# Optimization experiments

Measured on AMD Instinct MI355X. Metric: run time of the kernel, lower is better.

The kernel has to match this reference:

```python
import jax, jax.numpy as jnp
import numpy as np

FILTER_SIZE = 1024
NUM_HEADS = 16
D_HEAD = FILTER_SIZE // NUM_HEADS
LN_EPS = 1e-5


def setup_inputs() -> dict:
    key = jax.random.key(0)
    ks = jax.random.split(key, 10)
    B, T, D = 2, 2048, FILTER_SIZE
    s = 1.0 / np.sqrt(D)
    return {
        "x": jax.random.normal(ks[0], (B, T, D), dtype=jnp.float32),
        "Wq": jax.random.normal(ks[1], (D, D), dtype=jnp.float32) * s,
        "bq": jnp.zeros((D,), dtype=jnp.float32),
        "Wk": jax.random.normal(ks[2], (D, D), dtype=jnp.float32) * s,
        "bk": jnp.zeros((D,), dtype=jnp.float32),
        "Wv": jax.random.normal(ks[3], (D, D), dtype=jnp.float32) * s,
        "bv": jnp.zeros((D,), dtype=jnp.float32),
        "Wo": jax.random.normal(ks[4], (D, D), dtype=jnp.float32) * s,
        "bo": jnp.zeros((D,), dtype=jnp.float32),
        "gamma": jnp.ones((D,), dtype=jnp.float32),
        "beta": jnp.zeros((D,), dtype=jnp.float32),
    }


def reference(x, Wq, bq, Wk, bk, Wv, bv, Wo, bo, gamma, beta):
    B, T, D = x.shape
    H, Dh = NUM_HEADS, D_HEAD
    # Note: source splits features as (d_head, heads) with heads LAST.
    q = (x @ Wq.T + bq).reshape(B, T, Dh, H)
    k = (x @ Wk.T + bk).reshape(B, T, Dh, H)
    v = (x @ Wv.T + bv).reshape(B, T, Dh, H)
    scale = 1.0 / np.sqrt(Dh).astype(np.float32)
    # scores: (B, H, T, T)
    scores = jnp.einsum("bidh,bjdh->bhij", q, k) * scale
    attn = jax.nn.softmax(scores, axis=-1)  # dropout is identity in eval
    out = jnp.einsum("bhij,bjdh->bidh", attn, v)  # (B, T, Dh, H)
    out = out.reshape(B, T, D)  # matches permute(0,2,3,1).reshape in torch
    out = out @ Wo.T + bo
    out = out + x
    mu = jnp.mean(out, axis=-1, keepdims=True)
    var = jnp.var(out, axis=-1, keepdims=True)
    out = (out - mu) * jax.lax.rsqrt(var + LN_EPS) * gamma + beta
    return out
```

## Files before the change

kernel.cpp:

```cpp
#include <hip/hip_runtime.h>
#include <stdint.h>

#define T_SEQ 2048
#define D_MODEL 1024
#define NH 16
#define DH 64
#define NROWS 4096

typedef __bf16 bf16x8 __attribute__((ext_vector_type(8)));
typedef float floatx4 __attribute__((ext_vector_type(4)));
typedef short short4v __attribute__((ext_vector_type(4)));
typedef short short8v __attribute__((ext_vector_type(8)));

#define AS1 __attribute__((address_space(1)))
#define AS3 __attribute__((address_space(3)))

static __device__ __forceinline__ void gl2lds16(const unsigned short* g, unsigned short* s) {
    __builtin_amdgcn_global_load_lds((const AS1 unsigned int*)g, (AS3 unsigned int*)s, 16, 0, 0);
}

static __device__ __forceinline__ unsigned short f32_bf16(float f) {
    union { float f; unsigned int u; } c; c.f = f;
    unsigned int u = c.u;
    u = u + 0x7FFFu + ((u >> 16) & 1u);
    return (unsigned short)(u >> 16);
}

static __device__ __forceinline__ unsigned int pack2_bf16(float a, float b) {
    return (unsigned int)f32_bf16(a) | ((unsigned int)f32_bf16(b) << 16);
}

static __device__ __forceinline__ floatx4 mfma16(bf16x8 a, bf16x8 b, floatx4 c) {
    return __builtin_amdgcn_mfma_f32_16x16x32_bf16(a, b, c, 0, 0, 0);
}

static __device__ __forceinline__ floatx4 mfma16k16(short4v a, short4v b, floatx4 c) {
#if defined(__HIP_DEVICE_COMPILE__)
    return __builtin_amdgcn_mfma_f32_16x16x16bf16_1k(a, b, c, 0, 0, 0);
#else
    (void)a; (void)b;
    return c;
#endif
}

#define QSCALE 0.1803368801111204f
#define EXP2_SHIFT 10.0f
#define WAITCNT_VM(n) (0x0F70 | (n))

__global__ __launch_bounds__(256) void k_conv_all(const float* __restrict__ x,
                                                  const float* __restrict__ Wq,
                                                  const float* __restrict__ Wk,
                                                  const float* __restrict__ Wv,
                                                  const float* __restrict__ Wo,
                                                  unsigned short* __restrict__ x_bf,
                                                  unsigned short* __restrict__ wqkv_bf,
                                                  unsigned short* __restrict__ wo_bf) {
    int b = blockIdx.x, t = threadIdx.x;
    if (b < 4096) {
        int i = b * 1024 + t * 4;
        float4 v = *(const float4*)(x + i);
        uint2 o;
        o.x = pack2_bf16(v.x, v.y);
        o.y = pack2_bf16(v.z, v.w);
        *(uint2*)(x_bf + i) = o;
    } else if (b < 7168) {
        int idx = b - 4096;
        int tensor = idx >> 10, np = idx & 1023;
        const float* src = tensor == 0 ? Wq : tensor == 1 ? Wk : Wv;
        int f = (np & 63) * 16 + (np >> 6);
        int c = t * 4;
        float4 v = *(const float4*)(src + (long)f * D_MODEL + c);
        uint2 o;
        o.x = pack2_bf16(v.x, v.y);
        o.y = pack2_bf16(v.z, v.w);
        *(uint2*)(wqkv_bf + ((long)tensor * D_MODEL + np) * D_MODEL + c) = o;
    } else {
        int n = b - 7168;
        int fp = t * 4;
        const float* row = Wo + (long)n * D_MODEL;
        unsigned short o[4];
        #pragma unroll
        for (int k = 0; k < 4; k++) {
            int f = fp + k;
            o[k] = f32_bf16(row[(f & 63) * 16 + (f >> 6)]);
        }
        *(uint2*)(wo_bf + (long)n * D_MODEL + fp) = *(const uint2*)o;
    }
}

template <int BN, int MODE>
__global__ __launch_bounds__(256) void k_gemm(const unsigned short* __restrict__ A,
                                              const unsigned short* __restrict__ W,
                                              const float* __restrict__ b0,
                                              const float* __restrict__ b1,
                                              const float* __restrict__ b2,
                                              const float* __restrict__ resid,
                                              unsigned short* __restrict__ out_bf,
                                              unsigned short* __restrict__ vtg,
                                              float* __restrict__ out_f32) {
    constexpr int NT = BN / 32;
    constexpr int NCB = BN / 32;
    constexpr int NDMA = 4 + NCB;
    __shared__ unsigned short lds_a[2 * 128 * 64];
    __shared__ unsigned short lds_b[2 * BN * 64];
    const int tid = threadIdx.x;
    const int w = tid >> 6, l = tid & 63;
    const int lrow = l & 15, lq = l >> 4;
    const int wm = (w >> 1) * 64, wn = (w & 1) * (BN / 2);
    const int L = blockIdx.x;
    const int bx = (L & 7) * 4 + ((L >> 3) & 3);
    const int by = L >> 5;
    const long am0 = (long)bx * 128;
    const long wn0 = (long)by * BN;

    floatx4 acc[4][NT] = {};
    const int grow = l >> 3;
    const int gcol = ((l & 7) ^ grow) * 8;
    const int sw8 = (lrow & 7);

    auto stage = [&](int ki, int sel) {
        unsigned short* la = lds_a + sel * 8192;
        unsigned short* lb = lds_b + sel * (BN * 64);
        int k0 = ki * 64;
        #pragma unroll
        for (int c = 0; c < 4; c++) {
            int chunk = w * 4 + c;
            gl2lds16(A + (am0 + chunk * 8 + grow) * D_MODEL + k0 + gcol, la + chunk * 512);
        }
        #pragma unroll
        for (int c = 0; c < NCB; c++) {
            int chunk = w * NCB + c;
            gl2lds16(W + (wn0 + chunk * 8 + grow) * D_MODEL + k0 + gcol, lb + chunk * 512);
        }
    };

    stage(0, 0);

    for (int i = 0; i < 16; i++) {
        const int cur = i & 1;
        if (i < 15) {
            stage(i + 1, 1 - cur);
            __builtin_amdgcn_s_waitcnt(WAITCNT_VM(NDMA));
        } else {
            __builtin_amdgcn_s_waitcnt(WAITCNT_VM(0));
        }
        __builtin_amdgcn_s_barrier();

        const unsigned short* la = lds_a + cur * 8192;
        const unsigned short* lb = lds_b + cur * (BN * 64);
        bf16x8 af[4][2], bf[NT][2];
        #pragma unroll
        for (int mt = 0; mt < 4; mt++)
            #pragma unroll
            for (int ks = 0; ks < 2; ks++)
                af[mt][ks] = *(const bf16x8*)(la + (wm + mt * 16 + lrow) * 64 +
                                              (((ks * 4 + lq) ^ sw8) * 8));
        #pragma unroll
        for (int nt = 0; nt < NT; nt++)
            #pragma unroll
            for (int ks = 0; ks < 2; ks++)
                bf[nt][ks] = *(const bf16x8*)(lb + (wn + nt * 16 + lrow) * 64 +
                                              (((ks * 4 + lq) ^ sw8) * 8));
        #pragma unroll
        for (int mt = 0; mt < 4; mt++)
            #pragma unroll
            for (int nt = 0; nt < NT; nt++)
                #pragma unroll
                for (int ks = 0; ks < 2; ks++)
                    acc[mt][nt] = mfma16(af[mt][ks], bf[nt][ks], acc[mt][nt]);
        __builtin_amdgcn_s_barrier();
    }

    if (MODE == 0) {
        int tensor = by >> 3;
        int nbase = (by & 7) * 128;
        const float* bias = tensor == 0 ? b0 : tensor == 1 ? b1 : b2;
        float scale = tensor == 0 ? QSCALE : 1.0f;
        if (tensor < 2) {
            unsigned short* outt = out_bf + (size_t)tensor * (32u * T_SEQ * DH);
            #pragma unroll
            for (int mt = 0; mt < 4; mt++) {
                #pragma unroll
                for (int nt = 0; nt < NT; nt++) {
                    int n = nbase + wn + nt * 16 + lrow;
                    int h = n >> 6, d = n & 63;
                    float bb = bias[d * 16 + h];
                    #pragma unroll
                    for (int r = 0; r < 4; r++) {
                        int row = (int)am0 + wm + mt * 16 + lq * 4 + r;
                        float v = (acc[mt][nt][r] + bb) * scale;
                        int b = row >> 11, i = row & 2047;
                        long idx = ((long)(b * 16 + h) * T_SEQ + i) * DH + d;
                        outt[idx] = f32_bf16(v);
                    }
                }
            }
        } else {
            int row0 = (int)am0 + wm;
            int b = row0 >> 11;
            int blk = (row0 & 2047) >> 6;
            #pragma unroll
            for (int nt = 0; nt < NT; nt++) {
                int n = nbase + wn + nt * 16 + lrow;
                int h = n >> 6, d = n & 63;
                float bb = bias[d * 16 + h];
                long base = (((long)(b * 16 + h) * 64 + d) * 32 + blk) * 64;
                #pragma unroll
                for (int mt = 0; mt < 4; mt++) {
                    uint2 o;
                    o.x = pack2_bf16(acc[mt][nt][0] + bb, acc[mt][nt][1] + bb);
                    o.y = pack2_bf16(acc[mt][nt][2] + bb, acc[mt][nt][3] + bb);
                    *(uint2*)(vtg + base + lq * 16 + mt * 4) = o;
                }
            }
        }
    } else {
        #pragma unroll
        for (int mt = 0; mt < 4; mt++) {
            #pragma unroll
            for (int nt = 0; nt < NT; nt++) {
                int n = (int)wn0 + wn + nt * 16 + lrow;
                float bb = b0[n];
                #pragma unroll
                for (int r = 0; r < 4; r++) {
                    int row = (int)am0 + wm + mt * 16 + lq * 4 + r;
                    long idx = (long)row * D_MODEL + n;
                    out_f32[idx] = acc[mt][nt][r] + bb + resid[idx];
                }
            }
        }
    }
}

__global__ __launch_bounds__(256) void k_attn(const unsigned short* __restrict__ q_ws,
                                              const unsigned short* __restrict__ k_ws,
                                              const unsigned short* __restrict__ vtg,
                                              unsigned short* __restrict__ att) {
    __shared__ unsigned short kbuf[2 * 64 * 64];
    __shared__ unsigned short vbuf[2 * 64 * 64];
    const int tid = threadIdx.x;
    const int w = tid >> 6, l = tid & 63;
    const int lrow = l & 15, lq = l >> 4;
    const int sw = lrow & 7;
    const int L = blockIdx.x;
    const int bh = (L & 7) * 4 + ((L >> 3) & 3);
    const int i0 = (L >> 5) * 128;
    const unsigned short* kh = k_ws + (long)bh * T_SEQ * DH;
    const unsigned short* vh = vtg + (long)bh * 64 * T_SEQ;

    const int rl = l >> 3;
    const int gl = ((l & 7) ^ rl) * 8;

    bf16x8 qf[2][2];
    #pragma unroll
    for (int qt = 0; qt < 2; qt++) {
        const unsigned short* qp =
            q_ws + ((long)bh * T_SEQ + i0 + w * 32 + qt * 16 + lrow) * DH + lq * 8;
        qf[qt][0] = *(const bf16x8*)qp;
        qf[qt][1] = *(const bf16x8*)(qp + 32);
    }
    floatx4 o_acc[2][4] = {};
    floatx4 l_acc[2] = {};
    const short4v ones = {0x3F80, 0x3F80, 0x3F80, 0x3F80};

    auto stage = [&](int jt, int sel) {
        unsigned short* kd = kbuf + sel * 4096 + (w * 2) * 512;
        unsigned short* vd = vbuf + sel * 4096 + (w * 2) * 512;
        #pragma unroll
        for (int c = 0; c < 2; c++) {
            int row = w * 16 + c * 8 + rl;
            gl2lds16(kh + ((long)(jt * 64 + row)) * 64 + gl, kd + c * 512);
            gl2lds16(vh + ((long)row * 32 + jt) * 64 + gl, vd + c * 512);
        }
    };

    stage(0, 0);

    constexpr int NTILE = T_SEQ / 64;
    for (int jt = 0; jt < NTILE; jt++) {
        const int cur = jt & 1;
        if (jt < NTILE - 1) {
            stage(jt + 1, 1 - cur);
            __builtin_amdgcn_s_waitcnt(WAITCNT_VM(4));
        } else {
            __builtin_amdgcn_s_waitcnt(WAITCNT_VM(0));
        }
        __builtin_amdgcn_s_barrier();

        const unsigned short* kb_ = kbuf + cur * 4096;
        const unsigned short* vb_ = vbuf + cur * 4096;

        floatx4 s0[4], s1[4];
        #pragma unroll
        for (int nt = 0; nt < 4; nt++) {
            const unsigned short* kp = kb_ + (nt * 16 + lrow) * 64;
            bf16x8 ka = *(const bf16x8*)(kp + ((lq ^ sw) * 8));
            bf16x8 kb = *(const bf16x8*)(kp + (((lq + 4) ^ sw) * 8));
            floatx4 c0 = {-EXP2_SHIFT, -EXP2_SHIFT, -EXP2_SHIFT, -EXP2_SHIFT};
            floatx4 c1 = c0;
            c0 = mfma16(ka, qf[0][0], c0);
            c0 = mfma16(kb, qf[0][1], c0);
            c1 = mfma16(ka, qf[1][0], c1);
            c1 = mfma16(kb, qf[1][1], c1);
            s0[nt] = c0;
            s1[nt] = c1;
        }
        short4v pf0[4], pf1[4];
        #pragma unroll
        for (int nt = 0; nt < 4; nt++) {
            {
                float p0 = __builtin_amdgcn_exp2f(s0[nt][0]);
                float p1 = __builtin_amdgcn_exp2f(s0[nt][1]);
                float p2 = __builtin_amdgcn_exp2f(s0[nt][2]);
                float p3 = __builtin_amdgcn_exp2f(s0[nt][3]);
                uint2 pk;
                pk.x = __builtin_amdgcn_perm(__float_as_uint(p1), __float_as_uint(p0), 0x07060302);
                pk.y = __builtin_amdgcn_perm(__float_as_uint(p3), __float_as_uint(p2), 0x07060302);
                union { uint2 u; short4v s4; } cv; cv.u = pk;
                pf0[nt] = cv.s4;
                l_acc[0] = mfma16k16(ones, pf0[nt], l_acc[0]);
            }
            {
                float p0 = __builtin_amdgcn_exp2f(s1[nt][0]);
                float p1 = __builtin_amdgcn_exp2f(s1[nt][1]);
                float p2 = __builtin_amdgcn_exp2f(s1[nt][2]);
                float p3 = __builtin_amdgcn_exp2f(s1[nt][3]);
                uint2 pk;
                pk.x = __builtin_amdgcn_perm(__float_as_uint(p1), __float_as_uint(p0), 0x07060302);
                pk.y = __builtin_amdgcn_perm(__float_as_uint(p3), __float_as_uint(p2), 0x07060302);
                union { uint2 u; short4v s4; } cv; cv.u = pk;
                pf1[nt] = cv.s4;
                l_acc[1] = mfma16k16(ones, pf1[nt], l_acc[1]);
            }
        }
        #pragma unroll
        for (int dt = 0; dt < 4; dt++) {
            const unsigned short* vp = vb_ + (dt * 16 + lrow) * 64;
            short8v v01 = *(const short8v*)(vp + (((2 * lq) ^ sw) * 8));
            short8v v23 = *(const short8v*)(vp + (((2 * lq + 1) ^ sw) * 8));
            short4v va = __builtin_shufflevector(v01, v01, 0, 1, 2, 3);
            short4v vb = __builtin_shufflevector(v01, v01, 4, 5, 6, 7);
            short4v vc = __builtin_shufflevector(v23, v23, 0, 1, 2, 3);
            short4v vd = __builtin_shufflevector(v23, v23, 4, 5, 6, 7);
            o_acc[0][dt] = mfma16k16(va, pf0[0], o_acc[0][dt]);
            o_acc[0][dt] = mfma16k16(vb, pf0[1], o_acc[0][dt]);
            o_acc[0][dt] = mfma16k16(vc, pf0[2], o_acc[0][dt]);
            o_acc[0][dt] = mfma16k16(vd, pf0[3], o_acc[0][dt]);
            o_acc[1][dt] = mfma16k16(va, pf1[0], o_acc[1][dt]);
            o_acc[1][dt] = mfma16k16(vb, pf1[1], o_acc[1][dt]);
            o_acc[1][dt] = mfma16k16(vc, pf1[2], o_acc[1][dt]);
            o_acc[1][dt] = mfma16k16(vd, pf1[3], o_acc[1][dt]);
        }
        __builtin_amdgcn_s_barrier();
    }
    int h = bh & 15, b = bh >> 4;
    #pragma unroll
    for (int qt = 0; qt < 2; qt++) {
        float rl2 = 1.0f / l_acc[qt][0];
        int i = i0 + w * 32 + qt * 16 + lrow;
        unsigned short* orow = att + ((long)(b * T_SEQ + i)) * D_MODEL + h * 64;
        #pragma unroll
        for (int dt = 0; dt < 4; dt++) {
            uint2 o;
            o.x = pack2_bf16(o_acc[qt][dt][0] * rl2, o_acc[qt][dt][1] * rl2);
            o.y = pack2_bf16(o_acc[qt][dt][2] * rl2, o_acc[qt][dt][3] * rl2);
            *(uint2*)(orow + dt * 16 + lq * 4) = o;
        }
    }
}

__global__ __launch_bounds__(256) void k_ln(float* __restrict__ io,
                                            const float* __restrict__ gamma,
                                            const float* __restrict__ beta) {
    int row = blockIdx.x, t = threadIdx.x;
    float* p = io + (long)row * D_MODEL + t * 4;
    float4 v = *(float4*)p;
    float s = v.x + v.y + v.z + v.w;
    float ss = v.x * v.x + v.y * v.y + v.z * v.z + v.w * v.w;
    #pragma unroll
    for (int m = 1; m < 64; m <<= 1) {
        s += __shfl_xor(s, m);
        ss += __shfl_xor(ss, m);
    }
    __shared__ float red[8];
    if ((t & 63) == 0) { red[t >> 6] = s; red[4 + (t >> 6)] = ss; }
    __syncthreads();
    s = red[0] + red[1] + red[2] + red[3];
    ss = red[4] + red[5] + red[6] + red[7];
    float mu = s * (1.0f / 1024.0f);
    float var = ss * (1.0f / 1024.0f) - mu * mu;
    float rstd = rsqrtf(var + 1e-5f);
    float4 g = *(const float4*)(gamma + t * 4);
    float4 be = *(const float4*)(beta + t * 4);
    float4 o;
    o.x = (v.x - mu) * rstd * g.x + be.x;
    o.y = (v.y - mu) * rstd * g.y + be.y;
    o.z = (v.z - mu) * rstd * g.z + be.z;
    o.w = (v.w - mu) * rstd * g.w + be.w;
    *(float4*)p = o;
}

extern "C" void kernel_launch(void* const* d_in, const int* in_sizes, int n_in,
                              void* d_out, int out_size, void* d_ws, size_t ws_size,
                              hipStream_t stream) {
    const float* x = (const float*)d_in[0];
    const float* Wq = (const float*)d_in[1];
    const float* bq = (const float*)d_in[2];
    const float* Wk = (const float*)d_in[3];
    const float* bk = (const float*)d_in[4];
    const float* Wv = (const float*)d_in[5];
    const float* bv = (const float*)d_in[6];
    const float* Wo = (const float*)d_in[7];
    const float* bo = (const float*)d_in[8];
    const float* gamma = (const float*)d_in[9];
    const float* beta = (const float*)d_in[10];
    float* out = (float*)d_out;

    char* ws = (char*)d_ws;
    unsigned short* x_bf = (unsigned short*)(ws);
    unsigned short* wqkv_bf = (unsigned short*)(ws + ((size_t)8 << 20));
    unsigned short* wo_bf = (unsigned short*)(ws + ((size_t)14 << 20));
    unsigned short* qkv_ws = (unsigned short*)(ws + ((size_t)16 << 20));
    unsigned short* att = x_bf;

    unsigned short* q_ws = qkv_ws;
    unsigned short* k_ws = qkv_ws + (size_t)32 * T_SEQ * DH;
    unsigned short* vtg = qkv_ws + (size_t)64 * T_SEQ * DH;

    k_conv_all<<<8192, 256, 0, stream>>>(x, Wq, Wk, Wv, Wo, x_bf, wqkv_bf, wo_bf);

    k_gemm<128, 0><<<768, 256, 0, stream>>>(
        x_bf, wqkv_bf, bq, bk, bv, nullptr, qkv_ws, vtg, nullptr);

    k_attn<<<512, 256, 0, stream>>>(q_ws, k_ws, vtg, att);

    k_gemm<64, 1><<<512, 256, 0, stream>>>(
        att, wo_bf, bo, nullptr, nullptr, x, nullptr, nullptr, out);

    k_ln<<<NROWS, 256, 0, stream>>>(out, gamma, beta);
}
```

Before: 215.0 us.

## Software-pipeline attention loop so PV of previous tile overlaps QK/softmax of next

Restructures the attention inner loop into a skewed software pipeline: each step computes QK^T and exp/pack for tile t while issuing the P·V MFMAs for tile t-1, with K staged one tile ahead of V. Interleaving the exp2 (transcendental) work with the matrix ops is meant to hide softmax latency behind MFMA throughput. It doubles the P fragment registers (ping-pong buffers) and adds prologue/epilogue code. Register pressure and occupancy may suffer.

```diff
diff --git a/kernel.cpp b/kernel.cpp
--- a/kernel.cpp
+++ b/kernel.cpp
@@ -263,34 +263,24 @@
     floatx4 l_acc[2] = {};
     const short4v ones = {0x3F80, 0x3F80, 0x3F80, 0x3F80};
 
-    auto stage = [&](int jt, int sel) {
+    auto stage_k = [&](int jt, int sel) {
         unsigned short* kd = kbuf + sel * 4096 + (w * 2) * 512;
-        unsigned short* vd = vbuf + sel * 4096 + (w * 2) * 512;
         #pragma unroll
         for (int c = 0; c < 2; c++) {
             int row = w * 16 + c * 8 + rl;
             gl2lds16(kh + ((long)(jt * 64 + row)) * 64 + gl, kd + c * 512);
+        }
+    };
+    auto stage_v = [&](int jt, int sel) {
+        unsigned short* vd = vbuf + sel * 4096 + (w * 2) * 512;
+        #pragma unroll
+        for (int c = 0; c < 2; c++) {
+            int row = w * 16 + c * 8 + rl;
             gl2lds16(vh + ((long)row * 32 + jt) * 64 + gl, vd + c * 512);
         }
     };
 
-    stage(0, 0);
-
-    constexpr int NTILE = T_SEQ / 64;
-    for (int jt = 0; jt < NTILE; jt++) {
-        const int cur = jt & 1;
-        if (jt < NTILE - 1) {
-            stage(jt + 1, 1 - cur);
-            __builtin_amdgcn_s_waitcnt(WAITCNT_VM(4));
-        } else {
-            __builtin_amdgcn_s_waitcnt(WAITCNT_VM(0));
-        }
-        __builtin_amdgcn_s_barrier();
-
-        const unsigned short* kb_ = kbuf + cur * 4096;
-        const unsigned short* vb_ = vbuf + cur * 4096;
-
-        floatx4 s0[4], s1[4];
+    auto qk = [&](const unsigned short* kb_, floatx4 (&s0)[4], floatx4 (&s1)[4]) {
         #pragma unroll
         for (int nt = 0; nt < 4; nt++) {
             const unsigned short* kp = kb_ + (nt * 16 + lrow) * 64;
@@ -305,54 +295,99 @@
             s0[nt] = c0;
             s1[nt] = c1;
         }
-        short4v pf0[4], pf1[4];
-        #pragma unroll
-        for (int nt = 0; nt < 4; nt++) {
-            {
-                float p0 = __builtin_amdgcn_exp2f(s0[nt][0]);
-                float p1 = __builtin_amdgcn_exp2f(s0[nt][1]);
-                float p2 = __builtin_amdgcn_exp2f(s0[nt][2]);
-                float p3 = __builtin_amdgcn_exp2f(s0[nt][3]);
-                uint2 pk;
-                pk.x = __builtin_amdgcn_perm(__float_as_uint(p1), __float_as_uint(p0), 0x07060302);
-                pk.y = __builtin_amdgcn_perm(__float_as_uint(p3), __float_as_uint(p2), 0x07060302);
-                union { uint2 u; short4v s4; } cv; cv.u = pk;
-                pf0[nt] = cv.s4;
-                l_acc[0] = mfma16k16(ones, pf0[nt], l_acc[0]);
-            }
-            {
-                float p0 = __builtin_amdgcn_exp2f(s1[nt][0]);
-                float p1 = __builtin_amdgcn_exp2f(s1[nt][1]);
-                float p2 = __builtin_amdgcn_exp2f(s1[nt][2]);
-                float p3 = __builtin_amdgcn_exp2f(s1[nt][3]);
-                uint2 pk;
-                pk.x = __builtin_amdgcn_perm(__float_as_uint(p1), __float_as_uint(p0), 0x07060302);
-                pk.y = __builtin_amdgcn_perm(__float_as_uint(p3), __float_as_uint(p2), 0x07060302);
-                union { uint2 u; short4v s4; } cv; cv.u = pk;
-                pf1[nt] = cv.s4;
-                l_acc[1] = mfma16k16(ones, pf1[nt], l_acc[1]);
-            }
-        }
+    };
+
+    auto softpack = [&](floatx4 s, short4v& pf, int qt) {
+        float p0 = __builtin_amdgcn_exp2f(s[0]);
+        float p1 = __builtin_amdgcn_exp2f(s[1]);
+        float p2 = __builtin_amdgcn_exp2f(s[2]);
+        float p3 = __builtin_amdgcn_exp2f(s[3]);
+        uint2 pk;
+        pk.x = __builtin_amdgcn_perm(__float_as_uint(p1), __float_as_uint(p0), 0x07060302);
+        pk.y = __builtin_amdgcn_perm(__float_as_uint(p3), __float_as_uint(p2), 0x07060302);
+        union { uint2 u; short4v s4; } cv; cv.u = pk;
+        pf = cv.s4;
+        l_acc[qt] = mfma16k16(ones, pf, l_acc[qt]);
+    };
+
+    auto pv_dt = [&](const unsigned short* vb_, int dt,
+                     short4v (&p0)[4], short4v (&p1)[4]) {
+        const unsigned short* vp = vb_ + (dt * 16 + lrow) * 64;
+        short8v v01 = *(const short8v*)(vp + (((2 * lq) ^ sw) * 8));
+        short8v v23 = *(const short8v*)(vp + (((2 * lq + 1) ^ sw) * 8));
+        short4v va = __builtin_shufflevector(v01, v01, 0, 1, 2, 3);
+        short4v vb = __builtin_shufflevector(v01, v01, 4, 5, 6, 7);
+        short4v vc = __builtin_shufflevector(v23, v23, 0, 1, 2, 3);
+        short4v vd = __builtin_shufflevector(v23, v23, 4, 5, 6, 7);
+        o_acc[0][dt] = mfma16k16(va, p0[0], o_acc[0][dt]);
+        o_acc[0][dt] = mfma16k16(vb, p0[1], o_acc[0][dt]);
+        o_acc[0][dt] = mfma16k16(vc, p0[2], o_acc[0][dt]);
+        o_acc[0][dt] = mfma16k16(vd, p0[3], o_acc[0][dt]);
+        o_acc[1][dt] = mfma16k16(va, p1[0], o_acc[1][dt]);
+        o_acc[1][dt] = mfma16k16(vb, p1[1], o_acc[1][dt]);
+        o_acc[1][dt] = mfma16k16(vc, p1[2], o_acc[1][dt]);
+        o_acc[1][dt] = mfma16k16(vd, p1[3], o_acc[1][dt]);
+    };
+
+    auto tile_body = [&](const unsigned short* kb_, const unsigned short* vb_,
+                         short4v (&pp0)[4], short4v (&pp1)[4],
+                         short4v (&pc0)[4], short4v (&pc1)[4]) {
+        floatx4 s0[4], s1[4];
+        qk(kb_, s0, s1);
         #pragma unroll
         for (int dt = 0; dt < 4; dt++) {
-            const unsigned short* vp = vb_ + (dt * 16 + lrow) * 64;
-            short8v v01 = *(const short8v*)(vp + (((2 * lq) ^ sw) * 8));
-            short8v v23 = *(const short8v*)(vp + (((2 * lq + 1) ^ sw) * 8));
-            short4v va = __builtin_shufflevector(v01, v01, 0, 1, 2, 3);
-            short4v vb = __builtin_shufflevector(v01, v01, 4, 5, 6, 7);
-            short4v vc = __builtin_shufflevector(v23, v23, 0, 1, 2, 3);
-            short4v vd = __builtin_shufflevector(v23, v23, 4, 5, 6, 7);
-            o_acc[0][dt] = mfma16k16(va, pf0[0], o_acc[0][dt]);
-            o_acc[0][dt] = mfma16k16(vb, pf0[1], o_acc[0][dt]);
-            o_acc[0][dt] = mfma16k16(vc, pf0[2], o_acc[0][dt]);
-            o_acc[0][dt] = mfma16k16(vd, pf0[3], o_acc[0][dt]);
-            o_acc[1][dt] = mfma16k16(va, pf1[0], o_acc[1][dt]);
-            o_acc[1][dt] = mfma16k16(vb, pf1[1], o_acc[1][dt]);
-            o_acc[1][dt] = mfma16k16(vc, pf1[2], o_acc[1][dt]);
-            o_acc[1][dt] = mfma16k16(vd, pf1[3], o_acc[1][dt]);
-        }
-        __builtin_amdgcn_s_barrier();
-    }
+            pv_dt(vb_, dt, pp0, pp1);
+            softpack(s0[dt], pc0[dt], 0);
+            softpack(s1[dt], pc1[dt], 1);
+        }
+    };
+
+    short4v pA0[4], pA1[4], pB0[4], pB1[4];
+
+    stage_k(0, 0);
+    stage_k(1, 1);
+    stage_v(0, 0);
+    __builtin_amdgcn_s_waitcnt(WAITCNT_VM(4));
+    __builtin_amdgcn_s_barrier();
+    {
+        floatx4 s0[4], s1[4];
+        qk(kbuf, s0, s1);
+        #pragma unroll
+        for (int dt = 0; dt < 4; dt++) {
+            softpack(s0[dt], pA0[dt], 0);
+            softpack(s1[dt], pA1[dt], 1);
+        }
+    }
+    __builtin_amdgcn_s_barrier();
+
+    for (int t = 1; t < 31; t += 2) {
+        stage_k(t + 1, (t + 1) & 1);
+        stage_v(t, t & 1);
+        __builtin_amdgcn_s_waitcnt(WAITCNT_VM(4));
+        __builtin_amdgcn_s_barrier();
+        tile_body(kbuf + (t & 1) * 4096, vbuf + ((t - 1) & 1) * 4096,
+                  pA0, pA1, pB0, pB1);
+        __builtin_amdgcn_s_barrier();
+        stage_k(t + 2, t & 1);
+        stage_v(t + 1, (t + 1) & 1);
+        __builtin_amdgcn_s_waitcnt(WAITCNT_VM(4));
+        __builtin_amdgcn_s_barrier();
+        tile_body(kbuf + ((t + 1) & 1) * 4096, vbuf + (t & 1) * 4096,
+                  pB0, pB1, pA0, pA1);
+        __builtin_amdgcn_s_barrier();
+    }
+
+    stage_v(31, 1);
+    __builtin_amdgcn_s_waitcnt(WAITCNT_VM(2));
+    __builtin_amdgcn_s_barrier();
+    tile_body(kbuf + 4096, vbuf + 0, pA0, pA1, pB0, pB1);
+    __builtin_amdgcn_s_barrier();
+
+    __builtin_amdgcn_s_waitcnt(WAITCNT_VM(0));
+    __builtin_amdgcn_s_barrier();
+    #pragma unroll
+    for (int dt = 0; dt < 4; dt++) pv_dt(vbuf + 4096, dt, pB0, pB1);
+
     int h = bh & 15, b = bh >> 4;
     #pragma unroll
     for (int qt = 0; qt < 2; qt++) {
```

Result: no change. 213.6 us (-0.7%).
